# Kernel optimization log

Measured on AMD Instinct MI355X. Metric: run time of the kernel, lower is better.

The kernel has to match this reference:

```python
import jax, jax.numpy as jnp
import numpy as np

C = 300      # caption feature dim (word2vec)
OQK = 75     # in_dim // k = 300 // 4 -> query/key channels
H = 128      # adapt_img_hidden (base_proj dim)
LAT = 1024   # image latent size
EPS = 1e-5   # BatchNorm eps


def setup_inputs() -> dict:
    key = jax.random.key(0)
    ks = jax.random.split(key, 16)
    r = lambda i, shape, s=0.05: jax.random.normal(ks[i], shape, dtype=jnp.float32) * s
    return dict(
        img_embed=jax.random.normal(ks[0], (128, 36, LAT), dtype=jnp.float32),
        cap_embed=jax.random.normal(ks[1], (64, 32, C), dtype=jnp.float32),
        # adapt_img: Linear(1024, 128)
        adapt_W=r(2, (H, LAT)), adapt_b=jnp.zeros((H,), jnp.float32),
        # query ProjConv1d: kernel Linear(H, OQK*C), bias Linear(H, OQK), BatchNorm1d(OQK)
        qk_W=r(3, (OQK * C, H)), qk_b=r(4, (OQK * C,)),
        qb_W=r(5, (OQK, H)), qb_b=jnp.zeros((OQK,), jnp.float32),
        q_bn_s=jnp.ones((OQK,), jnp.float32), q_bn_b=jnp.zeros((OQK,), jnp.float32),
        # key ProjConv1d
        kk_W=r(6, (OQK * C, H)), kk_b=r(7, (OQK * C,)),
        kb_W=r(8, (OQK, H)), kb_b=jnp.zeros((OQK,), jnp.float32),
        k_bn_s=jnp.ones((OQK,), jnp.float32), k_bn_b=jnp.zeros((OQK,), jnp.float32),
        # value ProjConv1d: kernel Linear(H, C*C), bias Linear(H, C), BatchNorm1d(C)
        vk_W=r(9, (C * C, H)), vk_b=r(10, (C * C,)),
        vb_W=r(11, (C, H)), vb_b=jnp.zeros((C,), jnp.float32),
        v_bn_s=jnp.ones((C,), jnp.float32), v_bn_b=jnp.zeros((C,), jnp.float32),
        gamma=jnp.float32(0.5),  # residual attention gate (torch inits to 0; 0.5 exercises the path)
        # sim_proj MLP: 300 -> 512 -> 64 -> 1 with BatchNorm+ReLU (dropout = identity at eval)
        W1=r(12, (512, C)), b1=jnp.zeros((512,), jnp.float32),
        bn1_s=jnp.ones((512,), jnp.float32), bn1_b=jnp.zeros((512,), jnp.float32),
        W2=r(13, (64, 512)), b2=jnp.zeros((64,), jnp.float32),
        bn2_s=jnp.ones((64,), jnp.float32), bn2_b=jnp.zeros((64,), jnp.float32),
        W3=r(14, (1, 64)), b3=jnp.zeros((1,), jnp.float32),
    )


def _bn_kernel(kern, s, b):
    # torch: BatchNorm1d(out)(kernel.permute(1,0,2)) with kernel (out, in, ks=1)
    # -> per out-channel stats over the `in` axis (train-mode batch stats)
    mu = kern.mean(axis=1, keepdims=True)
    var = kern.var(axis=1, keepdims=True)
    return (kern - mu) / jnp.sqrt(var + EPS) * s[:, None] + b[:, None]


def _bn_batch(x, s, b):
    # BatchNorm1d over batch axis of (N, C) activations (train-mode stats)
    mu = x.mean(axis=0, keepdims=True)
    var = x.var(axis=0, keepdims=True)
    return (x - mu) / jnp.sqrt(var + EPS) * s + b


def reference(img_embed, cap_embed, adapt_W, adapt_b,
              qk_W, qk_b, qb_W, qb_b, q_bn_s, q_bn_b,
              kk_W, kk_b, kb_W, kb_b, k_bn_s, k_bn_b,
              vk_W, vk_b, vb_W, vb_b, v_bn_s, v_bn_b,
              gamma, W1, b1, bn1_s, bn1_b, W2, b2, bn2_s, bn2_b, W3, b3):
    cap = cap_embed.transpose(0, 2, 1)                      # (Bc, C, T)
    img_mean = img_embed.transpose(0, 2, 1).mean(-1)        # (Bi, LAT): mean over 36 regions
    base = img_mean @ adapt_W.T + adapt_b                   # (Bi, H)

    def per_image(bp):
        # hypernet-generated 1x1 conv kernels, batchnorm-normalized
        Kq = _bn_kernel((qk_W @ bp + qk_b).reshape(OQK, C), q_bn_s, q_bn_b)
        Kk = _bn_kernel((kk_W @ bp + kk_b).reshape(OQK, C), k_bn_s, k_bn_b)
        Kv = _bn_kernel((vk_W @ bp + vk_b).reshape(C, C), v_bn_s, v_bn_b)
        bq = qb_W @ bp + qb_b
        bk = kb_W @ bp + kb_b
        bv = vb_W @ bp + vb_b
        q = jnp.einsum('oc,nct->not', Kq, cap) + bq[:, None]    # (Bc, OQK, T)
        k = jnp.einsum('oc,nct->not', Kk, cap) + bk[:, None]    # (Bc, OQK, T)
        v = jnp.einsum('oc,nct->not', Kv, cap) + bv[:, None]    # (Bc, C, T)
        attn = jax.nn.softmax(jnp.einsum('not,nos->nts', q, k), axis=-1)  # (Bc, T, T)
        sa = jnp.einsum('ncs,nts->nct', v, attn)                # out = V @ attn^T
        x = (gamma * sa + cap).max(-1)                          # (Bc, C): max-pool over tokens
        h = jax.nn.relu(_bn_batch(x @ W1.T + b1, bn1_s, bn1_b))
        h = jax.nn.relu(_bn_batch(h @ W2.T + b2, bn2_s, bn2_b))
        return (h @ W3.T + b3)[:, 0]                            # (Bc,)

    return jax.vmap(per_image)(base)                            # (Bi, Bc)
```

## Files before the change

kernel.cpp:

```cpp
#include <hip/hip_runtime.h>
#include <math.h>

#define EPSB 1e-5f

static const long OFS_BASE  = 0;
static const long OFS_BALL  = 16384;
static const long OFS_MEAN  = 81920;
static const long OFS_CAPB  = 212992;
static const long OFS_RAWP  = 868352;
static const long OFS_X     = 15286272;
static const long OFS_H2    = 17743872;
static const long OFS_BASP  = 18268160;
static const long OFS_H1    = OFS_RAWP;

using bf16x8 = __attribute__((ext_vector_type(8))) __bf16;
using f32x4  = __attribute__((ext_vector_type(4))) float;
#define MFMA16(a, b, c) __builtin_amdgcn_mfma_f32_16x16x32_bf16(a, b, c, 0, 0, 0)

__device__ inline ushort f2bf(float f) {
  const unsigned u = __float_as_uint(f);
  return (ushort)((u + 0x7FFFu + ((u >> 16) & 1u)) >> 16);
}
__device__ inline float bf2f(ushort h) { return __uint_as_float(((unsigned)h) << 16); }

__global__ void k_mean(const float* __restrict__ img, float* __restrict__ mean) {
  const int idx = blockIdx.x * 256 + threadIdx.x;
  const int i = idx >> 10, l = idx & 1023;
  const float* p = img + (size_t)i * 36 * 1024 + l;
  float s = 0.f;
#pragma unroll
  for (int r = 0; r < 36; ++r) s += p[r * 1024];
  mean[idx] = s * (1.0f / 36.0f);
}

__global__ void k_base(const float* __restrict__ mean, const float* __restrict__ W,
                       const float* __restrict__ b, float* __restrict__ base) {
  __shared__ float m_s[1024];
  const int i = blockIdx.x, tid = threadIdx.x;
  for (int k = 0; k < 8; ++k) m_s[tid + 128 * k] = mean[i * 1024 + tid + 128 * k];
  __syncthreads();
  float acc = b[tid];
  const float* wr = W + (size_t)tid * 1024;
#pragma unroll 4
  for (int l = 0; l < 1024; ++l) acc = fmaf(m_s[l], wr[l], acc);
  base[i * 128 + tid] = acc;
}

__global__ void __launch_bounds__(256) k_basp(const float* __restrict__ base,
                                              ushort* __restrict__ basP) {
  const int half = blockIdx.x, tid = threadIdx.x;
  for (int m = 0; m < 8; ++m) {
    const int u = tid + 256 * m;
    const int ln = u & 63, unit = u >> 6;
    const int it = unit >> 3, ks = (unit >> 1) & 3, pl = unit & 1;
    const int i = half * 64 + it * 16 + (ln & 15);
    const int h = ks * 32 + (ln >> 4) * 8;
    ushort o8[8];
#pragma unroll
    for (int e = 0; e < 8; ++e) {
      const float v = base[(size_t)i * 128 + h + e];
      const ushort hi = f2bf(v);
      o8[e] = pl ? f2bf(v - bf2f(hi)) : hi;
    }
    uint4 pk;
    pk.x = (uint)o8[0] | ((uint)o8[1] << 16);
    pk.y = (uint)o8[2] | ((uint)o8[3] << 16);
    pk.z = (uint)o8[4] | ((uint)o8[5] << 16);
    pk.w = (uint)o8[6] | ((uint)o8[7] << 16);
    *reinterpret_cast<uint4*>(basP + (size_t)(half * 32 + unit) * 512 + ln * 8) = pk;
  }
}

__global__ void k_bias(const float* __restrict__ qbW, const float* __restrict__ qbb,
                       const float* __restrict__ kbW, const float* __restrict__ kbb,
                       const float* __restrict__ vbW, const float* __restrict__ vbb,
                       const float* __restrict__ base, float* __restrict__ ball) {
  __shared__ float bs[128];
  const int i = blockIdx.y, tid = threadIdx.x;
  if (tid < 128) bs[tid] = base[i * 128 + tid];
  __syncthreads();
  const int o = blockIdx.x * 256 + tid;
  if (o >= 512) return;
  const float* Wr = nullptr;
  float bb = 0.0f;
  if (o < 75)                   { Wr = qbW + (size_t)o * 128;         bb = qbb[o]; }
  else if (o >= 96 && o < 171)  { Wr = kbW + (size_t)(o - 96) * 128;  bb = kbb[o - 96]; }
  else if (o >= 192 && o < 492) { Wr = vbW + (size_t)(o - 192) * 128; bb = vbb[o - 192]; }
  float acc = 0.0f;
  if (Wr) {
#pragma unroll 4
    for (int h = 0; h < 128; ++h) acc = fmaf(Wr[h], bs[h], acc);
    acc += bb;
  }
  ball[i * 512 + o] = acc;
}

__global__ void __launch_bounds__(256) k_capp(const float* __restrict__ cap,
                                              ushort* __restrict__ capP) {
  __shared__ float ct[32 * 301];
  const int n = blockIdx.x, tid = threadIdx.x;
  const float* capn = cap + (size_t)n * 9600;
  {
    const int r = tid >> 3, c8 = tid & 7;
    for (int m = 0; m < 38; ++m) {
      const int c = c8 + 8 * m;
      if (c < 300) ct[r * 301 + c] = capn[r * 300 + c];
    }
  }
  __syncthreads();
  ushort* dst = capP + (size_t)n * 20480;
  for (int u = 0; u < 10; ++u) {
    const int ul = tid + 256 * u;
    const int unit = ul >> 6, lane = ul & 63;
    const int nt = unit / 20, rem = unit % 20;
    const int ks = rem >> 1, pl = rem & 1;
    const int kg = lane >> 4, lr = lane & 15;
    const int t = nt * 16 + lr;
    ushort o8[8];
#pragma unroll
    for (int e = 0; e < 8; ++e) {
      const int c = 32 * ks + 8 * kg + e;
      const float val = (c < 300) ? ct[t * 301 + c] : 0.f;
      const ushort hi = f2bf(val);
      o8[e] = pl ? f2bf(val - bf2f(hi)) : hi;
    }
    uint4 pk;
    pk.x = (uint)o8[0] | ((uint)o8[1] << 16);
    pk.y = (uint)o8[2] | ((uint)o8[3] << 16);
    pk.z = (uint)o8[4] | ((uint)o8[5] << 16);
    pk.w = (uint)o8[6] | ((uint)o8[7] << 16);
    *reinterpret_cast<uint4*>(dst + unit * 512 + lane * 8) = pk;
  }
}

__global__ void __launch_bounds__(256) k_hyp4(
    const float* __restrict__ qkW, const float* __restrict__ qkb,
    const float* __restrict__ kkW, const float* __restrict__ kkb,
    const float* __restrict__ vkW, const float* __restrict__ vkb,
    const float* __restrict__ qs, const float* __restrict__ qb,
    const float* __restrict__ ks_, const float* __restrict__ kb_,
    const float* __restrict__ vs, const float* __restrict__ vb,
    const ushort* __restrict__ basP, ushort* __restrict__ kall) {
  __shared__ float smem[19760];
  __shared__ float scl[64], shf[64];
  const int g = blockIdx.x, half = blockIdx.y, tid = threadIdx.x;
  const int i0g = half * 64;
  const int ot = g >> 4, lr = g & 15;
  const bool isV = (g >= 192);
  if ((g >= 80 && g < 96) || (g >= 176 && g < 192)) return;

  const float* Wb = nullptr;
  const float* bvec = nullptr;
  float bns = 0.f, bnb = 0.f;
  if (g < 75)                    { Wb = qkW + (size_t)g * 38400;          bvec = qkb + g * 300;          bns = qs[g];        bnb = qb[g]; }
  else if (g >= 96 && g < 171)   { Wb = kkW + (size_t)(g - 96) * 38400;   bvec = kkb + (g - 96) * 300;   bns = ks_[g - 96];  bnb = kb_[g - 96]; }
  else if (g >= 192 && g < 492)  { Wb = vkW + (size_t)(g - 192) * 38400;  bvec = vkb + (g - 192) * 300;  bns = vs[g - 192];  bnb = vb[g - 192]; }

  if (!Wb) {
    const uint4 z = make_uint4(0, 0, 0, 0);
    if (!isV) {
      for (int m = 0; m < 20; ++m) {
        const int idx = tid + 256 * m;
        const int ii = idx & 63, zz = idx >> 6;
        const int kg2 = zz & 3, pl = (zz >> 2) & 1, ks2 = zz >> 3;
        const size_t off = (size_t)(i0g + ii) * 225280 +
                           (size_t)(ot * 20 + ks2 * 2 + pl) * 512 + (kg2 * 16 + lr) * 8;
        *reinterpret_cast<uint4*>(kall + off) = z;
      }
    } else {
      for (int m = 0; m < 10; ++m) {
        const int idx = tid + 256 * m;
        const int ii = idx & 63, zz = idx >> 6;
        const int kg2 = zz & 3, ks2 = zz >> 2;
        const size_t off = (size_t)(i0g + ii) * 225280 +
                           (size_t)(240 + (ot - 12) * 10 + ks2) * 512 + (kg2 * 16 + lr) * 8;
        *reinterpret_cast<uint4*>(kall + off) = z;
      }
    }
    return;
  }

  const int lane = tid & 63, w = tid >> 6;
  const int lrow = lane & 15, kg = lane >> 4;
  ushort* Af = reinterpret_cast<ushort*>(smem + 9760);

  f32x4 acc[19];
#pragma unroll
  for (int ct = 0; ct < 19; ++ct) acc[ct] = (f32x4){0.f, 0.f, 0.f, 0.f};

  for (int hc = 0; hc < 4; ++hc) {
    __syncthreads();
    for (int m = 0; m < 10; ++m) {
      const int u = tid + 256 * m;
      if (u < 2432) {
        const int c = u >> 3, h4 = (u & 7) * 4;
        float4 wv = make_float4(0.f, 0.f, 0.f, 0.f);
        if (c < 300) wv = *reinterpret_cast<const float4*>(Wb + (size_t)c * 128 + hc * 32 + h4);
        smem[(h4 + 0) * 305 + c] = wv.x;
        smem[(h4 + 1) * 305 + c] = wv.y;
        smem[(h4 + 2) * 305 + c] = wv.z;
        smem[(h4 + 3) * 305 + c] = wv.w;
      }
    }
    __syncthreads();
    for (int m = 0; m < 5; ++m) {
      const int u = tid + 256 * m;
      if (u < 1216) {
        const int ln = u & 63, ct = u >> 6;
        const int cc = ct * 16 + (ln & 15);
        const int hb = (ln >> 4) * 8;
        ushort h8[8], l8[8];
#pragma unroll
        for (int e = 0; e < 8; ++e) {
          const float v = smem[(hb + e) * 305 + cc];
          const ushort hi = f2bf(v);
          h8[e] = hi;
          l8[e] = f2bf(v - bf2f(hi));
        }
        uint4 ph, pl4;
        ph.x = (uint)h8[0] | ((uint)h8[1] << 16);
        ph.y = (uint)h8[2] | ((uint)h8[3] << 16);
        ph.z = (uint)h8[4] | ((uint)h8[5] << 16);
        ph.w = (uint)h8[6] | ((uint)h8[7] << 16);
        pl4.x = (uint)l8[0] | ((uint)l8[1] << 16);
        pl4.y = (uint)l8[2] | ((uint)l8[3] << 16);
        pl4.z = (uint)l8[4] | ((uint)l8[5] << 16);
        pl4.w = (uint)l8[6] | ((uint)l8[7] << 16);
        *reinterpret_cast<uint4*>(&Af[(ct * 2 + 0) * 512 + ln * 8]) = ph;
        *reinterpret_cast<uint4*>(&Af[(ct * 2 + 1) * 512 + ln * 8]) = pl4;
      }
    }
    const bf16x8 Bh = *reinterpret_cast<const bf16x8*>(
        basP + (size_t)(half * 32 + w * 8 + hc * 2 + 0) * 512 + lane * 8);
    const bf16x8 Bl = *reinterpret_cast<const bf16x8*>(
        basP + (size_t)(half * 32 + w * 8 + hc * 2 + 1) * 512 + lane * 8);
    __syncthreads();
#pragma unroll
    for (int ct = 0; ct < 19; ++ct) {
      const bf16x8 Ah = *reinterpret_cast<const bf16x8*>(&Af[(ct * 2 + 0) * 512 + lane * 8]);
      const bf16x8 Al = *reinterpret_cast<const bf16x8*>(&Af[(ct * 2 + 1) * 512 + lane * 8]);
      acc[ct] = MFMA16(Ah, Bh, acc[ct]);
      acc[ct] = MFMA16(Ah, Bl, acc[ct]);
      acc[ct] = MFMA16(Al, Bh, acc[ct]);
    }
  }
  __syncthreads();
#pragma unroll
  for (int ct = 0; ct < 19; ++ct)
#pragma unroll
    for (int r = 0; r < 4; ++r) {
      const int c = ct * 16 + kg * 4 + r;
      if (c < 300) smem[c * 65 + w * 16 + lrow] = acc[ct][r] + bvec[c];
    }
  __syncthreads();
  {
    const int si = tid >> 2, p = tid & 3;
    float s1 = 0.f, s2 = 0.f;
    for (int c = p; c < 300; c += 4) {
      const float x = smem[c * 65 + si];
      s1 += x;
      s2 += x * x;
    }
    s1 += __shfl_xor(s1, 1); s2 += __shfl_xor(s2, 1);
    s1 += __shfl_xor(s1, 2); s2 += __shfl_xor(s2, 2);
    const float mu = s1 * (1.0f / 300.0f);
    const float var = s2 * (1.0f / 300.0f) - mu * mu;
    const float scale = bns / sqrtf(var + EPSB);
    if (p == 0) { scl[si] = scale; shf[si] = bnb - mu * scale; }
  }
  __syncthreads();
  if (!isV) {
    for (int m = 0; m < 20; ++m) {
      const int idx = tid + 256 * m;
      const int ii = idx & 63, zz = idx >> 6;
      const int kg2 = zz & 3, pl = (zz >> 2) & 1, ks2 = zz >> 3;
      const float sc = scl[ii], sh = shf[ii];
      ushort o8[8];
#pragma unroll
      for (int e = 0; e < 8; ++e) {
        const int c = ks2 * 32 + kg2 * 8 + e;
        float val = 0.f;
        if (c < 300) val = fmaf(smem[c * 65 + ii], sc, sh);
        const ushort hi = f2bf(val);
        o8[e] = pl ? f2bf(val - bf2f(hi)) : hi;
      }
      uint4 pk;
      pk.x = (uint)o8[0] | ((uint)o8[1] << 16);
      pk.y = (uint)o8[2] | ((uint)o8[3] << 16);
      pk.z = (uint)o8[4] | ((uint)o8[5] << 16);
      pk.w = (uint)o8[6] | ((uint)o8[7] << 16);
      const size_t off = (size_t)(i0g + ii) * 225280 +
                         (size_t)(ot * 20 + ks2 * 2 + pl) * 512 + (kg2 * 16 + lr) * 8;
      *reinterpret_cast<uint4*>(kall + off) = pk;
    }
  } else {
    for (int m = 0; m < 10; ++m) {
      const int idx = tid + 256 * m;
      const int ii = idx & 63, zz = idx >> 6;
      const int kg2 = zz & 3, ks2 = zz >> 2;
      const float sc = scl[ii], sh = shf[ii];
      ushort o8[8];
#pragma unroll
      for (int e = 0; e < 8; ++e) {
        const int c = ks2 * 32 + kg2 * 8 + e;
        float val = 0.f;
        if (c < 300) val = fmaf(smem[c * 65 + ii], sc, sh);
        o8[e] = f2bf(val);
      }
      uint4 pk;
      pk.x = (uint)o8[0] | ((uint)o8[1] << 16);
      pk.y = (uint)o8[2] | ((uint)o8[3] << 16);
      pk.z = (uint)o8[4] | ((uint)o8[5] << 16);
      pk.w = (uint)o8[6] | ((uint)o8[7] << 16);
      const size_t off = (size_t)(i0g + ii) * 225280 +
                         (size_t)(240 + (ot - 12) * 10 + ks2) * 512 + (kg2 * 16 + lr) * 8;
      *reinterpret_cast<uint4*>(kall + off) = pk;
    }
  }
}

__global__ void __launch_bounds__(256, 4) k_attn11(
    const float* __restrict__ cap, const ushort* __restrict__ kall,
    const ushort* __restrict__ capP, const float* __restrict__ ball,
    const float* __restrict__ gptr, float* __restrict__ x_all) {
  __shared__ ushort qkp[24 * 512];
  __shared__ float sc_s[32 * 36];
  __shared__ ushort at_p[2 * 2 * 64 * 8];
  const int bid = blockIdx.x;
  const int xcd = bid & 7, q = bid >> 3;
  const int i = xcd * 16 + (q >> 6), n = q & 63;
  const int tid = threadIdx.x;
  const int lane = tid & 63, w = tid >> 6;
  const int lrow = lane & 15, kg = lane >> 4;
  const float gamma = gptr[0];
  const ushort* kpL = kall + (size_t)i * 225280 + lane * 8;
  const ushort* cpL = capP + (size_t)n * 20480 + lane * 8;
  const float* bal = ball + i * 512;
  const bool oddw = (w & 1);

  {
    f32x4 acc[3][2];
#pragma unroll
    for (int a = 0; a < 3; ++a)
#pragma unroll
      for (int b2 = 0; b2 < 2; ++b2) acc[a][b2] = (f32x4){0.f, 0.f, 0.f, 0.f};
    bf16x8 AhA[3], AlA[3], AhB[3], AlB[3];
#pragma unroll
    for (int mt = 0; mt < 3; ++mt)
      if (!oddw || mt < 2) {
        const ushort* p = kpL + (size_t)((w * 3 + mt) * 20) * 512;
        AhA[mt] = *reinterpret_cast<const bf16x8*>(p);
        AlA[mt] = *reinterpret_cast<const bf16x8*>(p + 512);
      }
#pragma unroll
    for (int kp = 0; kp < 5; ++kp) {
      {
        const int ks = 2 * kp;
        bf16x8 Bh[2], Bl[2];
#pragma unroll
        for (int nt = 0; nt < 2; ++nt) {
          const ushort* p = cpL + (size_t)(nt * 20 + ks * 2) * 512;
          Bh[nt] = *reinterpret_cast<const bf16x8*>(p);
          Bl[nt] = *reinterpret_cast<const bf16x8*>(p + 512);
        }
#pragma unroll
        for (int mt = 0; mt < 3; ++mt)
          if (!oddw || mt < 2) {
            const ushort* p = kpL + (size_t)((w * 3 + mt) * 20 + (ks + 1) * 2) * 512;
            AhB[mt] = *reinterpret_cast<const bf16x8*>(p);
            AlB[mt] = *reinterpret_cast<const bf16x8*>(p + 512);
          }
#pragma unroll
        for (int mt = 0; mt < 3; ++mt)
          if (!oddw || mt < 2)
#pragma unroll
            for (int nt = 0; nt < 2; ++nt) {
              acc[mt][nt] = MFMA16(AhA[mt], Bh[nt], acc[mt][nt]);
              acc[mt][nt] = MFMA16(AhA[mt], Bl[nt], acc[mt][nt]);
              acc[mt][nt] = MFMA16(AlA[mt], Bh[nt], acc[mt][nt]);
            }
      }
      {
        const int ks = 2 * kp + 1;
        bf16x8 Bh[2], Bl[2];
#pragma unroll
        for (int nt = 0; nt < 2; ++nt) {
          const ushort* p = cpL + (size_t)(nt * 20 + ks * 2) * 512;
          Bh[nt] = *reinterpret_cast<const bf16x8*>(p);
          Bl[nt] = *reinterpret_cast<const bf16x8*>(p + 512);
        }
        if (kp < 4) {
#pragma unroll
          for (int mt = 0; mt < 3; ++mt)
            if (!oddw || mt < 2) {
              const ushort* p = kpL + (size_t)((w * 3 + mt) * 20 + (ks + 1) * 2) * 512;
              AhA[mt] = *reinterpret_cast<const bf16x8*>(p);
              AlA[mt] = *reinterpret_cast<const bf16x8*>(p + 512);
            }
        }
#pragma unroll
        for (int mt = 0; mt < 3; ++mt)
          if (!oddw || mt < 2)
#pragma unroll
            for (int nt = 0; nt < 2; ++nt) {
              acc[mt][nt] = MFMA16(AhB[mt], Bh[nt], acc[mt][nt]);
              acc[mt][nt] = MFMA16(AhB[mt], Bl[nt], acc[mt][nt]);
              acc[mt][nt] = MFMA16(AlB[mt], Bh[nt], acc[mt][nt]);
            }
      }
    }
#pragma unroll
    for (int mt = 0; mt < 3; ++mt)
#pragma unroll
      for (int nt = 0; nt < 2; ++nt)
#pragma unroll
        for (int r = 0; r < 4; ++r) {
          const int og = w * 48 + mt * 16 + kg * 4 + r;
          const float val = acc[mt][nt][r] + bal[og];
          const ushort hi = f2bf(val);
          const ushort lo = f2bf(val - bf2f(hi));
          const int os = (w < 2) ? og : og - 96;
          const int ub = ((w < 2) ? 0 : 12) + nt * 6 + (os >> 5) * 2;
          const int lp = ((os & 31) >> 3) * 16 + lrow;
          const int e = os & 7;
          qkp[(ub + 0) * 512 + lp * 8 + e] = hi;
          qkp[(ub + 1) * 512 + lp * 8 + e] = lo;
        }
  }
  __syncthreads();

  {
    const int tt = w >> 1, st = w & 1;
    bf16x8 Aq[3][2], Bk[3][2];
#pragma unroll
    for (int k3 = 0; k3 < 3; ++k3)
#pragma unroll
      for (int pl = 0; pl < 2; ++pl) {
        Aq[k3][pl] = *reinterpret_cast<const bf16x8*>(&qkp[(tt * 6 + k3 * 2 + pl) * 512 + lane * 8]);
        Bk[k3][pl] = *reinterpret_cast<const bf16x8*>(&qkp[(12 + st * 6 + k3 * 2 + pl) * 512 + lane * 8]);
      }
    f32x4 D = (f32x4){0.f, 0.f, 0.f, 0.f};
#pragma unroll
    for (int k3 = 0; k3 < 3; ++k3) {
      D = MFMA16(Aq[k3][0], Bk[k3][0], D);
      D = MFMA16(Aq[k3][0], Bk[k3][1], D);
      D = MFMA16(Aq[k3][1], Bk[k3][0], D);
      D = MFMA16(Aq[k3][1], Bk[k3][1], D);
    }
#pragma unroll
    for (int r = 0; r < 4; ++r)
      sc_s[(tt * 16 + kg * 4 + r) * 36 + st * 16 + lrow] = D[r];
  }
  __syncthreads();

  {
    const int sg = tid & 7, tq = tid >> 3;
    const int s0 = sg * 4;
    const float4 sv = *reinterpret_cast<const float4*>(&sc_s[tq * 36 + s0]);
    float sc[4] = {sv.x, sv.y, sv.z, sv.w};
    float m = fmaxf(fmaxf(sc[0], sc[1]), fmaxf(sc[2], sc[3]));
    m = fmaxf(m, __shfl_xor(m, 1));
    m = fmaxf(m, __shfl_xor(m, 2));
    m = fmaxf(m, __shfl_xor(m, 4));
    float ev[4], ssum = 0.f;
#pragma unroll
    for (int u = 0; u < 4; ++u) { ev[u] = expf(sc[u] - m); ssum += ev[u]; }
    ssum += __shfl_xor(ssum, 1);
    ssum += __shfl_xor(ssum, 2);
    ssum += __shfl_xor(ssum, 4);
    const float inv = 1.0f / ssum;
    const int tt = tq >> 4, lrp = tq & 15, kgp = sg >> 1, eb = (sg & 1) * 4;
    ushort h4[4], l4[4];
#pragma unroll
    for (int u = 0; u < 4; ++u) {
      const float val = ev[u] * inv;
      const ushort hi = f2bf(val);
      h4[u] = hi;
      l4[u] = f2bf(val - bf2f(hi));
    }
    uint2 ph, pl2;
    ph.x = (uint)h4[0] | ((uint)h4[1] << 16);
    ph.y = (uint)h4[2] | ((uint)h4[3] << 16);
    pl2.x = (uint)l4[0] | ((uint)l4[1] << 16);
    pl2.y = (uint)l4[2] | ((uint)l4[3] << 16);
    *reinterpret_cast<uint2*>(&at_p[((tt * 2 + 0) * 64 + kgp * 16 + lrp) * 8 + eb]) = ph;
    *reinterpret_cast<uint2*>(&at_p[((tt * 2 + 1) * 64 + kgp * 16 + lrp) * 8 + eb]) = pl2;
  }
  __syncthreads();

  ushort* vt = qkp;
#pragma unroll
  for (int ch = 0; ch < 2; ++ch) {
    const int TB = 12 + ch * 12;
    const int RB = TB * 16;
    const int nmt = ch ? 2 : 3;
    f32x4 vacc[3][2];
#pragma unroll
    for (int a = 0; a < 3; ++a)
#pragma unroll
      for (int b2 = 0; b2 < 2; ++b2) vacc[a][b2] = (f32x4){0.f, 0.f, 0.f, 0.f};
    bf16x8 AvA[3], AvB[3];
    for (int mi = 0; mi < nmt; ++mi)
      AvA[mi] = *reinterpret_cast<const bf16x8*>(
          kpL + (size_t)(240 + (TB - 12 + w + mi * 4) * 10) * 512);
#pragma unroll
    for (int kp = 0; kp < 5; ++kp) {
      {
        const int ks = 2 * kp;
        bf16x8 Bh[2];
#pragma unroll
        for (int nt = 0; nt < 2; ++nt)
          Bh[nt] = *reinterpret_cast<const bf16x8*>(cpL + (size_t)(nt * 20 + ks * 2) * 512);
        for (int mi = 0; mi < nmt; ++mi)
          AvB[mi] = *reinterpret_cast<const bf16x8*>(
              kpL + (size_t)(240 + (TB - 12 + w + mi * 4) * 10 + ks + 1) * 512);
        for (int mi = 0; mi < nmt; ++mi)
#pragma unroll
          for (int nt = 0; nt < 2; ++nt)
            vacc[mi][nt] = MFMA16(AvA[mi], Bh[nt], vacc[mi][nt]);
      }
      {
        const int ks = 2 * kp + 1;
        bf16x8 Bh[2];
#pragma unroll
        for (int nt = 0; nt < 2; ++nt)
          Bh[nt] = *reinterpret_cast<const bf16x8*>(cpL + (size_t)(nt * 20 + ks * 2) * 512);
        if (kp < 4) {
          for (int mi = 0; mi < nmt; ++mi)
            AvA[mi] = *reinterpret_cast<const bf16x8*>(
                kpL + (size_t)(240 + (TB - 12 + w + mi * 4) * 10 + ks + 1) * 512);
        }
        for (int mi = 0; mi < nmt; ++mi)
#pragma unroll
          for (int nt = 0; nt < 2; ++nt)
            vacc[mi][nt] = MFMA16(AvB[mi], Bh[nt], vacc[mi][nt]);
      }
    }
    if (ch) __syncthreads();
    for (int mi = 0; mi < nmt; ++mi) {
      const int tile = w + mi * 4;
#pragma unroll
      for (int nt = 0; nt < 2; ++nt) {
        const int kgp = nt * 2 + (lrow >> 3), ee = lrow & 7;
#pragma unroll
        for (int r = 0; r < 4; ++r) {
          const int vl = tile * 16 + kg * 4 + r;
          const float val = vacc[mi][nt][r] + bal[RB + vl];
          const ushort hi = f2bf(val);
          vt[((tile * 2 + 0) * 64 + kgp * 16 + kg * 4 + r) * 8 + ee] = hi;
          vt[((tile * 2 + 1) * 64 + kgp * 16 + kg * 4 + r) * 8 + ee] = f2bf(val - bf2f(hi));
        }
      }
    }
    __syncthreads();
    {
      bf16x8 ah[2], al[2];
#pragma unroll
      for (int tt = 0; tt < 2; ++tt) {
        ah[tt] = *reinterpret_cast<const bf16x8*>(&at_p[((tt * 2 + 0) * 64 + lane) * 8]);
        al[tt] = *reinterpret_cast<const bf16x8*>(&at_p[((tt * 2 + 1) * 64 + lane) * 8]);
      }
      const int npw = ch ? 2 : 3;
      for (int j = 0; j < npw; ++j) {
        const int ct = w * npw + j;
        const int c0 = ch * 192 + ct * 16 + (lane >> 4) * 4;
        const bf16x8 vh  = *reinterpret_cast<const bf16x8*>(&vt[((ct * 2 + 0) * 64 + lane) * 8]);
        const bf16x8 vl8 = *reinterpret_cast<const bf16x8*>(&vt[((ct * 2 + 1) * 64 + lane) * 8]);
        f32x4 a0 = (f32x4){0.f, 0.f, 0.f, 0.f}, a1 = (f32x4){0.f, 0.f, 0.f, 0.f};
        a0 = MFMA16(vh, ah[0], a0);
        a0 = MFMA16(vh, al[0], a0);
        a0 = MFMA16(vl8, ah[0], a0);
        a1 = MFMA16(vh, ah[1], a1);
        a1 = MFMA16(vh, al[1], a1);
        a1 = MFMA16(vl8, ah[1], a1);
        if (c0 < 300) {
          const int t0 = lane & 15;
          const float4 c4a = *reinterpret_cast<const float4*>(&cap[(size_t)n * 9600 + t0 * 300 + c0]);
          const float4 c4b = *reinterpret_cast<const float4*>(&cap[(size_t)n * 9600 + (t0 + 16) * 300 + c0]);
          float mx[4];
          mx[0] = fmaxf(fmaf(gamma, a0[0], c4a.x), fmaf(gamma, a1[0], c4b.x));
          mx[1] = fmaxf(fmaf(gamma, a0[1], c4a.y), fmaf(gamma, a1[1], c4b.y));
          mx[2] = fmaxf(fmaf(gamma, a0[2], c4a.z), fmaf(gamma, a1[2], c4b.z));
          mx[3] = fmaxf(fmaf(gamma, a0[3], c4a.w), fmaf(gamma, a1[3], c4b.w));
#pragma unroll
          for (int mmask = 1; mmask < 16; mmask <<= 1)
#pragma unroll
            for (int r = 0; r < 4; ++r) mx[r] = fmaxf(mx[r], __shfl_xor(mx[r], mmask));
          if ((lane & 15) == 0)
            *reinterpret_cast<float4*>(&x_all[((size_t)i * 64 + n) * 300 + c0]) =
                make_float4(mx[0], mx[1], mx[2], mx[3]);
        }
      }
    }
  }
}

__global__ void __launch_bounds__(256, 4) k_h1b(
    const float* __restrict__ x_all, const float* __restrict__ W1,
    const float* __restrict__ b1, const float* __restrict__ bn1s,
    const float* __restrict__ bn1b, float* __restrict__ h1) {
  __shared__ float xt[32 * 68];
  __shared__ float wt[32 * 132];
  __shared__ float sc1[128], sh1[128];
  const int ec = blockIdx.x, i = blockIdx.y, tid = threadIdx.x;
  const int e0c = ec * 128;
  const int eg = tid & 15, ng = tid >> 4;
  const int e0 = eg * 8, n0 = ng * 4;
  float acc[4][8] = {};
  for (int cb = 0; cb < 10; ++cb) {
    const int c0 = cb * 32;
    __syncthreads();
    for (int k = 0; k < 8; ++k) {
      const int idx = tid + 256 * k;
      const int nn = idx >> 5, cl = idx & 31;
      const int c = c0 + cl;
      xt[cl * 68 + nn] = (c < 300) ? x_all[((size_t)i * 64 + nn) * 300 + c] : 0.0f;
    }
    for (int k = 0; k < 16; ++k) {
      const int idx = tid + 256 * k;
      const int ee = idx >> 5, cl = idx & 31;
      const int c = c0 + cl;
      wt[cl * 132 + ee] = (c < 300) ? W1[(size_t)(e0c + ee) * 300 + c] : 0.0f;
    }
    __syncthreads();
#pragma unroll 4
    for (int cl = 0; cl < 32; ++cl) {
      const float4 xv = *reinterpret_cast<const float4*>(&xt[cl * 68 + n0]);
      const float4 wa = *reinterpret_cast<const float4*>(&wt[cl * 132 + e0]);
      const float4 wb = *reinterpret_cast<const float4*>(&wt[cl * 132 + e0 + 4]);
      const float xv4[4] = {xv.x, xv.y, xv.z, xv.w};
      const float wv8[8] = {wa.x, wa.y, wa.z, wa.w, wb.x, wb.y, wb.z, wb.w};
#pragma unroll
      for (int u = 0; u < 4; ++u)
#pragma unroll
        for (int v = 0; v < 8; ++v) acc[u][v] = fmaf(xv4[u], wv8[v], acc[u][v]);
    }
  }
  float b1v[8];
#pragma unroll
  for (int v = 0; v < 8; ++v) b1v[v] = b1[e0c + e0 + v];
  float val[4][8];
#pragma unroll
  for (int u = 0; u < 4; ++u)
#pragma unroll
    for (int v = 0; v < 8; ++v) val[u][v] = acc[u][v] + b1v[v];
  __syncthreads();
  float* ps1 = xt;
  float* ps2 = wt;
#pragma unroll
  for (int v = 0; v < 8; ++v) {
    float su = 0.f, sq = 0.f;
#pragma unroll
    for (int u = 0; u < 4; ++u) { su += val[u][v]; sq += val[u][v] * val[u][v]; }
    ps1[ng * 132 + e0 + v] = su;
    ps2[ng * 132 + e0 + v] = sq;
  }
  __syncthreads();
  if (tid < 128) {
    const int e = tid;
    float s1 = 0.f, s2 = 0.f;
#pragma unroll 4
    for (int gq = 0; gq < 16; ++gq) { s1 += ps1[gq * 132 + e]; s2 += ps2[gq * 132 + e]; }
    const float mu = s1 * (1.0f / 64.0f);
    const float var = s2 * (1.0f / 64.0f) - mu * mu;
    const float scale = bn1s[e0c + e] / sqrtf(var + EPSB);
    sc1[e] = scale;
    sh1[e] = bn1b[e0c + e] - mu * scale;
  }
  __syncthreads();
#pragma unroll
  for (int u = 0; u < 4; ++u) {
    float o8[8];
#pragma unroll
    for (int v = 0; v < 8; ++v)
      o8[v] = fmaxf(fmaf(val[u][v], sc1[e0 + v], sh1[e0 + v]), 0.0f);
    float* dst = h1 + ((size_t)i * 64 + n0 + u) * 512 + e0c + e0;
    *reinterpret_cast<float4*>(dst) = make_float4(o8[0], o8[1], o8[2], o8[3]);
    *reinterpret_cast<float4*>(dst + 4) = make_float4(o8[4], o8[5], o8[6], o8[7]);
  }
}

__global__ void __launch_bounds__(256) k_h2(
    const float* __restrict__ h1, const float* __restrict__ W2,
    const float* __restrict__ b2, float* __restrict__ h2buf) {
  __shared__ float h1s[32 * 517];
  const int jn = blockIdx.x, i = blockIdx.y, tid = threadIdx.x;
  const int bn = jn * 32;
  for (int m = 0; m < 64; ++m) {
    const int idx = tid + 256 * m;
    h1s[(idx >> 9) * 517 + (idx & 511)] = h1[((size_t)i * 64 + bn) * 512 + idx];
  }
  __syncthreads();
  const int dg = tid & 15, ng2 = tid >> 4;
  const int d0 = dg * 4, n0 = ng2 * 2;
  float a0[4] = {}, a1[4] = {};
#pragma unroll 4
  for (int e = 0; e < 512; ++e) {
    const float h0 = h1s[n0 * 517 + e];
    const float h1v = h1s[(n0 + 1) * 517 + e];
#pragma unroll
    for (int v = 0; v < 4; ++v) {
      const float wv = W2[(size_t)(d0 + v) * 512 + e];
      a0[v] = fmaf(h0, wv, a0[v]);
      a1[v] = fmaf(h1v, wv, a1[v]);
    }
  }
  const float4 bb = *reinterpret_cast<const float4*>(&b2[d0]);
  float* dst0 = h2buf + ((size_t)i * 64 + bn + n0) * 64 + d0;
  *reinterpret_cast<float4*>(dst0) = make_float4(a0[0] + bb.x, a0[1] + bb.y, a0[2] + bb.z, a0[3] + bb.w);
  *reinterpret_cast<float4*>(dst0 + 64) = make_float4(a1[0] + bb.x, a1[1] + bb.y, a1[2] + bb.z, a1[3] + bb.w);
}

__global__ void __launch_bounds__(256) k_out(
    const float* __restrict__ h2buf, const float* __restrict__ bn2s,
    const float* __restrict__ bn2b, const float* __restrict__ W3,
    const float* __restrict__ b3, float* __restrict__ out) {
  __shared__ float h2s[64 * 65];
  const int i = blockIdx.x, tid = threadIdx.x;
  for (int m = 0; m < 16; ++m) {
    const int idx = tid + 256 * m;
    h2s[(idx >> 6) * 65 + (idx & 63)] = h2buf[(size_t)i * 4096 + idx];
  }
  __syncthreads();
  if (tid < 64) {
    const int d = tid;
    float s1 = 0.f, s2 = 0.f;
    for (int nn = 0; nn < 64; ++nn) {
      const float v = h2s[nn * 65 + d];
      s1 += v;
      s2 += v * v;
    }
    const float mu = s1 * (1.0f / 64.0f);
    const float var = s2 * (1.0f / 64.0f) - mu * mu;
    const float scale = bn2s[d] / sqrtf(var + EPSB);
    const float shift = bn2b[d] - mu * scale;
    for (int nn = 0; nn < 64; ++nn)
      h2s[nn * 65 + d] = fmaxf(fmaf(h2s[nn * 65 + d], scale, shift), 0.0f);
  }
  __syncthreads();
  if (tid < 64) {
    const int nn = tid;
    float acc = b3[0];
    for (int d = 0; d < 64; ++d) acc = fmaf(h2s[nn * 65 + d], W3[d], acc);
    out[i * 64 + nn] = acc;
  }
}

extern "C" void kernel_launch(void* const* d_in, const int* in_sizes, int n_in,
                              void* d_out, int out_size, void* d_ws, size_t ws_size,
                              hipStream_t stream) {
  const float* img  = (const float*)d_in[0];
  const float* cap  = (const float*)d_in[1];
  const float* adW  = (const float*)d_in[2];
  const float* adb  = (const float*)d_in[3];
  const float* qkW  = (const float*)d_in[4];
  const float* qkb  = (const float*)d_in[5];
  const float* qbW  = (const float*)d_in[6];
  const float* qbb  = (const float*)d_in[7];
  const float* qbns = (const float*)d_in[8];
  const float* qbnb = (const float*)d_in[9];
  const float* kkW  = (const float*)d_in[10];
  const float* kkb  = (const float*)d_in[11];
  const float* kbW  = (const float*)d_in[12];
  const float* kbb  = (const float*)d_in[13];
  const float* kbns = (const float*)d_in[14];
  const float* kbnb = (const float*)d_in[15];
  const float* vkW  = (const float*)d_in[16];
  const float* vkb  = (const float*)d_in[17];
  const float* vbW  = (const float*)d_in[18];
  const float* vbb  = (const float*)d_in[19];
  const float* vbns = (const float*)d_in[20];
  const float* vbnb = (const float*)d_in[21];
  const float* gamma= (const float*)d_in[22];
  const float* W1   = (const float*)d_in[23];
  const float* b1   = (const float*)d_in[24];
  const float* bn1s = (const float*)d_in[25];
  const float* bn1b = (const float*)d_in[26];
  const float* W2   = (const float*)d_in[27];
  const float* b2   = (const float*)d_in[28];
  const float* bn2s = (const float*)d_in[29];
  const float* bn2b = (const float*)d_in[30];
  const float* W3   = (const float*)d_in[31];
  const float* b3   = (const float*)d_in[32];

  float* ws    = (float*)d_ws;
  float* base  = ws + OFS_BASE;
  float* ball  = ws + OFS_BALL;
  float* mean  = ws + OFS_MEAN;
  ushort* capP = (ushort*)(ws + OFS_CAPB);
  ushort* kall = (ushort*)(ws + OFS_RAWP);
  float* x_all = ws + OFS_X;
  float* h2buf = ws + OFS_H2;
  ushort* basP = (ushort*)(ws + OFS_BASP);
  float* h1    = ws + OFS_H1;
  float* out   = (float*)d_out;

  k_mean<<<512, 256, 0, stream>>>(img, mean);
  k_base<<<128, 128, 0, stream>>>(mean, adW, adb, base);
  k_basp<<<2, 256, 0, stream>>>(base, basP);
  k_bias<<<dim3(2, 128), 256, 0, stream>>>(qbW, qbb, kbW, kbb, vbW, vbb, base, ball);
  k_capp<<<64, 256, 0, stream>>>(cap, capP);
  k_hyp4<<<dim3(512, 2), 256, 0, stream>>>(qkW, qkb, kkW, kkb, vkW, vkb,
                                           qbns, qbnb, kbns, kbnb, vbns, vbnb, basP, kall);
  k_attn11<<<8192, 256, 0, stream>>>(cap, kall, capP, ball, gamma, x_all);
  k_h1b<<<dim3(4, 128), 256, 0, stream>>>(x_all, W1, b1, bn1s, bn1b, h1);
  k_h2<<<dim3(2, 128), 256, 0, stream>>>(h1, W2, b2, h2buf);
  k_out<<<128, 256, 0, stream>>>(h2buf, bn2s, bn2b, W3, b3, out);
}
```

Before: 516.4 us.

## Fuse prep kernels and vectorize LDS stores in attention by swapping MFMA operands

Merges the mean and base projection into one kernel, and the bias, caption-pack and base-pack kernels into one multi-role launch, cutting the launch count from five to two. In the attention kernel, the packing of the q/k/v results into shared memory now writes four bf16 values at a time (uint2) instead of one scalar ushort store each. For V, the MFMA operand order is swapped so the accumulator layout matches the shared-memory layout and the bias load becomes a single value per tile. The operand swap changes which lanes own which outputs, and the store indexing must match that exactly for results to stay correct.

```diff
diff --git a/kernel.cpp b/kernel.cpp
--- a/kernel.cpp
+++ b/kernel.cpp
@@ -5,7 +5,6 @@
 
 static const long OFS_BASE  = 0;
 static const long OFS_BALL  = 16384;
-static const long OFS_MEAN  = 81920;
 static const long OFS_CAPB  = 212992;
 static const long OFS_RAWP  = 868352;
 static const long OFS_X     = 15286272;
@@ -23,113 +22,116 @@
 }
 __device__ inline float bf2f(ushort h) { return __uint_as_float(((unsigned)h) << 16); }
 
-__global__ void k_mean(const float* __restrict__ img, float* __restrict__ mean) {
-  const int idx = blockIdx.x * 256 + threadIdx.x;
-  const int i = idx >> 10, l = idx & 1023;
-  const float* p = img + (size_t)i * 36 * 1024 + l;
-  float s = 0.f;
-#pragma unroll
-  for (int r = 0; r < 36; ++r) s += p[r * 1024];
-  mean[idx] = s * (1.0f / 36.0f);
+__global__ void __launch_bounds__(256) k_mb(const float* __restrict__ img,
+                                            const float* __restrict__ W,
+                                            const float* __restrict__ b,
+                                            float* __restrict__ base) {
+  __shared__ float m_s[1024];
+  __shared__ float part[128];
+  const int i = blockIdx.x, tid = threadIdx.x;
+#pragma unroll
+  for (int lc = 0; lc < 4; ++lc) {
+    const int l = lc * 256 + tid;
+    const float* p = img + (size_t)i * 36864 + l;
+    float s = 0.f;
+#pragma unroll
+    for (int r = 0; r < 36; ++r) s += p[r * 1024];
+    m_s[l] = s * (1.0f / 36.0f);
+  }
+  __syncthreads();
+  const int o = tid & 127, hk = tid >> 7;
+  const float* wr = W + (size_t)o * 1024 + hk * 512;
+  const float* ms = m_s + hk * 512;
+  float acc = 0.f;
+#pragma unroll 4
+  for (int l = 0; l < 512; ++l) acc = fmaf(ms[l], wr[l], acc);
+  if (hk) part[o] = acc;
+  __syncthreads();
+  if (!hk) base[i * 128 + o] = acc + part[o] + b[o];
 }
 
-__global__ void k_base(const float* __restrict__ mean, const float* __restrict__ W,
-                       const float* __restrict__ b, float* __restrict__ base) {
-  __shared__ float m_s[1024];
-  const int i = blockIdx.x, tid = threadIdx.x;
-  for (int k = 0; k < 8; ++k) m_s[tid + 128 * k] = mean[i * 1024 + tid + 128 * k];
-  __syncthreads();
-  float acc = b[tid];
-  const float* wr = W + (size_t)tid * 1024;
+__global__ void __launch_bounds__(256) k_prep(
+    const float* __restrict__ qbW, const float* __restrict__ qbb,
+    const float* __restrict__ kbW, const float* __restrict__ kbb,
+    const float* __restrict__ vbW, const float* __restrict__ vbb,
+    const float* __restrict__ base, float* __restrict__ ball,
+    const float* __restrict__ cap, ushort* __restrict__ capP,
+    ushort* __restrict__ basP) {
+  __shared__ float shm[32 * 301];
+  const int bid = blockIdx.x, tid = threadIdx.x;
+  if (bid < 256) {
+    const int i = bid >> 1;
+    if (tid < 128) shm[tid] = base[i * 128 + tid];
+    __syncthreads();
+    const int o = (bid & 1) * 256 + tid;
+    const float* Wr = nullptr;
+    float bb = 0.0f;
+    if (o < 75)                   { Wr = qbW + (size_t)o * 128;         bb = qbb[o]; }
+    else if (o >= 96 && o < 171)  { Wr = kbW + (size_t)(o - 96) * 128;  bb = kbb[o - 96]; }
+    else if (o >= 192 && o < 492) { Wr = vbW + (size_t)(o - 192) * 128; bb = vbb[o - 192]; }
+    float acc = 0.0f;
+    if (Wr) {
 #pragma unroll 4
-  for (int l = 0; l < 1024; ++l) acc = fmaf(m_s[l], wr[l], acc);
-  base[i * 128 + tid] = acc;
-}
-
-__global__ void __launch_bounds__(256) k_basp(const float* __restrict__ base,
-                                              ushort* __restrict__ basP) {
-  const int half = blockIdx.x, tid = threadIdx.x;
-  for (int m = 0; m < 8; ++m) {
-    const int u = tid + 256 * m;
-    const int ln = u & 63, unit = u >> 6;
-    const int it = unit >> 3, ks = (unit >> 1) & 3, pl = unit & 1;
-    const int i = half * 64 + it * 16 + (ln & 15);
-    const int h = ks * 32 + (ln >> 4) * 8;
-    ushort o8[8];
-#pragma unroll
-    for (int e = 0; e < 8; ++e) {
-      const float v = base[(size_t)i * 128 + h + e];
-      const ushort hi = f2bf(v);
-      o8[e] = pl ? f2bf(v - bf2f(hi)) : hi;
-    }
-    uint4 pk;
-    pk.x = (uint)o8[0] | ((uint)o8[1] << 16);
-    pk.y = (uint)o8[2] | ((uint)o8[3] << 16);
-    pk.z = (uint)o8[4] | ((uint)o8[5] << 16);
-    pk.w = (uint)o8[6] | ((uint)o8[7] << 16);
-    *reinterpret_cast<uint4*>(basP + (size_t)(half * 32 + unit) * 512 + ln * 8) = pk;
-  }
-}
-
-__global__ void k_bias(const float* __restrict__ qbW, const float* __restrict__ qbb,
-                       const float* __restrict__ kbW, const float* __restrict__ kbb,
-                       const float* __restrict__ vbW, const float* __restrict__ vbb,
-                       const float* __restrict__ base, float* __restrict__ ball) {
-  __shared__ float bs[128];
-  const int i = blockIdx.y, tid = threadIdx.x;
-  if (tid < 128) bs[tid] = base[i * 128 + tid];
-  __syncthreads();
-  const int o = blockIdx.x * 256 + tid;
-  if (o >= 512) return;
-  const float* Wr = nullptr;
-  float bb = 0.0f;
-  if (o < 75)                   { Wr = qbW + (size_t)o * 128;         bb = qbb[o]; }
-  else if (o >= 96 && o < 171)  { Wr = kbW + (size_t)(o - 96) * 128;  bb = kbb[o - 96]; }
-  else if (o >= 192 && o < 492) { Wr = vbW + (size_t)(o - 192) * 128; bb = vbb[o - 192]; }
-  float acc = 0.0f;
-  if (Wr) {
-#pragma unroll 4
-    for (int h = 0; h < 128; ++h) acc = fmaf(Wr[h], bs[h], acc);
-    acc += bb;
-  }
-  ball[i * 512 + o] = acc;
-}
-
-__global__ void __launch_bounds__(256) k_capp(const float* __restrict__ cap,
-                                              ushort* __restrict__ capP) {
-  __shared__ float ct[32 * 301];
-  const int n = blockIdx.x, tid = threadIdx.x;
-  const float* capn = cap + (size_t)n * 9600;
-  {
-    const int r = tid >> 3, c8 = tid & 7;
-    for (int m = 0; m < 38; ++m) {
-      const int c = c8 + 8 * m;
-      if (c < 300) ct[r * 301 + c] = capn[r * 300 + c];
-    }
-  }
-  __syncthreads();
-  ushort* dst = capP + (size_t)n * 20480;
-  for (int u = 0; u < 10; ++u) {
-    const int ul = tid + 256 * u;
-    const int unit = ul >> 6, lane = ul & 63;
-    const int nt = unit / 20, rem = unit % 20;
-    const int ks = rem >> 1, pl = rem & 1;
-    const int kg = lane >> 4, lr = lane & 15;
-    const int t = nt * 16 + lr;
-    ushort o8[8];
-#pragma unroll
-    for (int e = 0; e < 8; ++e) {
-      const int c = 32 * ks + 8 * kg + e;
-      const float val = (c < 300) ? ct[t * 301 + c] : 0.f;
-      const ushort hi = f2bf(val);
-      o8[e] = pl ? f2bf(val - bf2f(hi)) : hi;
-    }
-    uint4 pk;
-    pk.x = (uint)o8[0] | ((uint)o8[1] << 16);
-    pk.y = (uint)o8[2] | ((uint)o8[3] << 16);
-    pk.z = (uint)o8[4] | ((uint)o8[5] << 16);
-    pk.w = (uint)o8[6] | ((uint)o8[7] << 16);
-    *reinterpret_cast<uint4*>(dst + unit * 512 + lane * 8) = pk;
+      for (int h = 0; h < 128; ++h) acc = fmaf(Wr[h], shm[h], acc);
+      acc += bb;
+    }
+    ball[i * 512 + o] = acc;
+  } else if (bid < 320) {
+    const int n = bid - 256;
+    const float* capn = cap + (size_t)n * 9600;
+    {
+      const int r = tid >> 3, c8 = tid & 7;
+      for (int m = 0; m < 38; ++m) {
+        const int c = c8 + 8 * m;
+        if (c < 300) shm[r * 301 + c] = capn[r * 300 + c];
+      }
+    }
+    __syncthreads();
+    ushort* dst = capP + (size_t)n * 20480;
+    for (int u = 0; u < 10; ++u) {
+      const int ul = tid + 256 * u;
+      const int unit = ul >> 6, lane = ul & 63;
+      const int nt = unit / 20, rem = unit % 20;
+      const int ks = rem >> 1, pl = rem & 1;
+      const int kg = lane >> 4, lr = lane & 15;
+      const int t = nt * 16 + lr;
+      ushort o8[8];
+#pragma unroll
+      for (int e = 0; e < 8; ++e) {
+        const int c = 32 * ks + 8 * kg + e;
+        const float val = (c < 300) ? shm[t * 301 + c] : 0.f;
+        const ushort hi = f2bf(val);
+        o8[e] = pl ? f2bf(val - bf2f(hi)) : hi;
+      }
+      uint4 pk;
+      pk.x = (uint)o8[0] | ((uint)o8[1] << 16);
+      pk.y = (uint)o8[2] | ((uint)o8[3] << 16);
+      pk.z = (uint)o8[4] | ((uint)o8[5] << 16);
+      pk.w = (uint)o8[6] | ((uint)o8[7] << 16);
+      *reinterpret_cast<uint4*>(dst + unit * 512 + lane * 8) = pk;
+    }
+  } else {
+    const int half = bid - 320;
+    for (int m = 0; m < 8; ++m) {
+      const int u = tid + 256 * m;
+      const int ln = u & 63, unit = u >> 6;
+      const int it = unit >> 3, ks = (unit >> 1) & 3, pl = unit & 1;
+      const int i = half * 64 + it * 16 + (ln & 15);
+      const int h = ks * 32 + (ln >> 4) * 8;
+      ushort o8[8];
+#pragma unroll
+      for (int e = 0; e < 8; ++e) {
+        const float v = base[(size_t)i * 128 + h + e];
+        const ushort hi = f2bf(v);
+        o8[e] = pl ? f2bf(v - bf2f(hi)) : hi;
+      }
+      uint4 pk;
+      pk.x = (uint)o8[0] | ((uint)o8[1] << 16);
+      pk.y = (uint)o8[2] | ((uint)o8[3] << 16);
+      pk.z = (uint)o8[4] | ((uint)o8[5] << 16);
+      pk.w = (uint)o8[6] | ((uint)o8[7] << 16);
+      *reinterpret_cast<uint4*>(basP + (size_t)(half * 32 + unit) * 512 + ln * 8) = pk;
+    }
   }
 }
 
@@ -319,7 +321,7 @@
   }
 }
 
-__global__ void __launch_bounds__(256, 4) k_attn11(
+__global__ void __launch_bounds__(256, 4) k_attn12(
     const float* __restrict__ cap, const ushort* __restrict__ kall,
     const ushort* __restrict__ capP, const float* __restrict__ ball,
     const float* __restrict__ gptr, float* __restrict__ x_all) {
@@ -412,20 +414,28 @@
 #pragma unroll
     for (int mt = 0; mt < 3; ++mt)
 #pragma unroll
-      for (int nt = 0; nt < 2; ++nt)
+      for (int nt = 0; nt < 2; ++nt) {
+        const int og0 = w * 48 + mt * 16 + kg * 4;
+        const int os0 = (w < 2) ? og0 : og0 - 96;
+        const int ub = ((w < 2) ? 0 : 12) + nt * 6 + (os0 >> 5) * 2;
+        const int lp = ((os0 & 31) >> 3) * 16 + lrow;
+        const int e0 = os0 & 7;
+        ushort h4[4], l4[4];
 #pragma unroll
         for (int r = 0; r < 4; ++r) {
-          const int og = w * 48 + mt * 16 + kg * 4 + r;
-          const float val = acc[mt][nt][r] + bal[og];
+          const float val = acc[mt][nt][r] + bal[og0 + r];
           const ushort hi = f2bf(val);
-          const ushort lo = f2bf(val - bf2f(hi));
-          const int os = (w < 2) ? og : og - 96;
-          const int ub = ((w < 2) ? 0 : 12) + nt * 6 + (os >> 5) * 2;
-          const int lp = ((os & 31) >> 3) * 16 + lrow;
-          const int e = os & 7;
-          qkp[(ub + 0) * 512 + lp * 8 + e] = hi;
-          qkp[(ub + 1) * 512 + lp * 8 + e] = lo;
+          h4[r] = hi;
+          l4[r] = f2bf(val - bf2f(hi));
         }
+        uint2 ph, pl2;
+        ph.x = (uint)h4[0] | ((uint)h4[1] << 16);
+        ph.y = (uint)h4[2] | ((uint)h4[3] << 16);
+        pl2.x = (uint)l4[0] | ((uint)l4[1] << 16);
+        pl2.y = (uint)l4[2] | ((uint)l4[3] << 16);
+        *reinterpret_cast<uint2*>(&qkp[(ub + 0) * 512 + lp * 8 + e0]) = ph;
+        *reinterpret_cast<uint2*>(&qkp[(ub + 1) * 512 + lp * 8 + e0]) = pl2;
+      }
   }
   __syncthreads();
 
@@ -507,24 +517,24 @@
     for (int kp = 0; kp < 5; ++kp) {
       {
         const int ks = 2 * kp;
-        bf16x8 Bh[2];
+        bf16x8 Ch[2];
 #pragma unroll
         for (int nt = 0; nt < 2; ++nt)
-          Bh[nt] = *reinterpret_cast<const bf16x8*>(cpL + (size_t)(nt * 20 + ks * 2) * 512);
+          Ch[nt] = *reinterpret_cast<const bf16x8*>(cpL + (size_t)(nt * 20 + ks * 2) * 512);
         for (int mi = 0; mi < nmt; ++mi)
           AvB[mi] = *reinterpret_cast<const bf16x8*>(
               kpL + (size_t)(240 + (TB - 12 + w + mi * 4) * 10 + ks + 1) * 512);
         for (int mi = 0; mi < nmt; ++mi)
 #pragma unroll
           for (int nt = 0; nt < 2; ++nt)
-            vacc[mi][nt] = MFMA16(AvA[mi], Bh[nt], vacc[mi][nt]);
+            vacc[mi][nt] = MFMA16(Ch[nt], AvA[mi], vacc[mi][nt]);
       }
       {
         const int ks = 2 * kp + 1;
-        bf16x8 Bh[2];
+        bf16x8 Ch[2];
 #pragma unroll
         for (int nt = 0; nt < 2; ++nt)
-          Bh[nt] = *reinterpret_cast<const bf16x8*>(cpL + (size_t)(nt * 20 + ks * 2) * 512);
+          Ch[nt] = *reinterpret_cast<const bf16x8*>(cpL + (size_t)(nt * 20 + ks * 2) * 512);
         if (kp < 4) {
           for (int mi = 0; mi < nmt; ++mi)
             AvA[mi] = *reinterpret_cast<const bf16x8*>(
@@ -533,23 +543,32 @@
         for (int mi = 0; mi < nmt; ++mi)
 #pragma unroll
           for (int nt = 0; nt < 2; ++nt)
-            vacc[mi][nt] = MFMA16(AvB[mi], Bh[nt], vacc[mi][nt]);
+            vacc[mi][nt] = MFMA16(Ch[nt], AvB[mi], vacc[mi][nt]);
       }
     }
     if (ch) __syncthreads();
     for (int mi = 0; mi < nmt; ++mi) {
       const int tile = w + mi * 4;
+      const float bb = bal[RB + tile * 16 + lrow];
 #pragma unroll
       for (int nt = 0; nt < 2; ++nt) {
-        const int kgp = nt * 2 + (lrow >> 3), ee = lrow & 7;
+        const int lpv = (nt * 2 + (kg >> 1)) * 16 + lrow;
+        const int e0v = (kg & 1) * 4;
+        ushort h4[4], l4[4];
 #pragma unroll
         for (int r = 0; r < 4; ++r) {
-          const int vl = tile * 16 + kg * 4 + r;
-          const float val = vacc[mi][nt][r] + bal[RB + vl];
+          const float val = vacc[mi][nt][r] + bb;
           const ushort hi = f2bf(val);
-          vt[((tile * 2 + 0) * 64 + kgp * 16 + kg * 4 + r) * 8 + ee] = hi;
-          vt[((tile * 2 + 1) * 64 + kgp * 16 + kg * 4 + r) * 8 + ee] = f2bf(val - bf2f(hi));
+          h4[r] = hi;
+          l4[r] = f2bf(val - bf2f(hi));
         }
+        uint2 ph, pl2;
+        ph.x = (uint)h4[0] | ((uint)h4[1] << 16);
+        ph.y = (uint)h4[2] | ((uint)h4[3] << 16);
+        pl2.x = (uint)l4[0] | ((uint)l4[1] << 16);
+        pl2.y = (uint)l4[2] | ((uint)l4[3] << 16);
+        *reinterpret_cast<uint2*>(&vt[((tile * 2 + 0) * 64 + lpv) * 8 + e0v]) = ph;
+        *reinterpret_cast<uint2*>(&vt[((tile * 2 + 1) * 64 + lpv) * 8 + e0v]) = pl2;
       }
     }
     __syncthreads();
@@ -786,7 +805,6 @@
   float* ws    = (float*)d_ws;
   float* base  = ws + OFS_BASE;
   float* ball  = ws + OFS_BALL;
-  float* mean  = ws + OFS_MEAN;
   ushort* capP = (ushort*)(ws + OFS_CAPB);
   ushort* kall = (ushort*)(ws + OFS_RAWP);
   float* x_all = ws + OFS_X;
@@ -795,14 +813,11 @@
   float* h1    = ws + OFS_H1;
   float* out   = (float*)d_out;
 
-  k_mean<<<512, 256, 0, stream>>>(img, mean);
-  k_base<<<128, 128, 0, stream>>>(mean, adW, adb, base);
-  k_basp<<<2, 256, 0, stream>>>(base, basP);
-  k_bias<<<dim3(2, 128), 256, 0, stream>>>(qbW, qbb, kbW, kbb, vbW, vbb, base, ball);
-  k_capp<<<64, 256, 0, stream>>>(cap, capP);
+  k_mb<<<128, 256, 0, stream>>>(img, adW, adb, base);
+  k_prep<<<322, 256, 0, stream>>>(qbW, qbb, kbW, kbb, vbW, vbb, base, ball, cap, capP, basP);
   k_hyp4<<<dim3(512, 2), 256, 0, stream>>>(qkW, qkb, kkW, kkb, vkW, vkb,
                                            qbns, qbnb, kbns, kbnb, vbns, vbnb, basP, kall);
-  k_attn11<<<8192, 256, 0, stream>>>(cap, kall, capP, ball, gamma, x_all);
+  k_attn12<<<8192, 256, 0, stream>>>(cap, kall, capP, ball, gamma, x_all);
   k_h1b<<<dim3(4, 128), 256, 0, stream>>>(x_all, W1, b1, bn1s, bn1b, h1);
   k_h2<<<dim3(2, 128), 256, 0, stream>>>(h1, W2, b2, h2buf);
   k_out<<<128, 256, 0, stream>>>(h2buf, bn2s, bn2b, W3, b3, out);
```

New measurement: 486.0 us. -5.9%, faster.
